# Kernel tuning notes

Hardware: AMD Instinct MI355X
Metric: run time of the kernel (lower is better)

## Reference

```python
import jax, jax.numpy as jnp
import numpy as np

CHUNK_SIZE = 2048
LOCAL_WINDOW = 384
CHUNK_LEN = CHUNK_SIZE - LOCAL_WINDOW  # 1664
N_HEADS = 16
N_KV_HEADS = 4
HEAD_DIM = 128
HIDDEN = 2048
SEQ = 3 * CHUNK_LEN  # 4992
NEG_INF = -1e9


def _cos_sin(positions, dim=HEAD_DIM, base=10000.0):
    inv = 1.0 / (base ** (np.arange(0, dim, 2, dtype=np.float64) / dim))
    freqs = np.outer(np.asarray(positions, np.float64), inv)
    emb = np.concatenate([freqs, freqs], axis=-1)
    return jnp.asarray(np.cos(emb), jnp.float32), jnp.asarray(np.sin(emb), jnp.float32)


def setup_inputs() -> dict:
    key = jax.random.key(0)
    ks = jax.random.split(key, 5)
    hidden_states = jax.random.normal(ks[0], (1, SEQ, HIDDEN), jnp.float32) * 0.02
    position_ids = jnp.arange(SEQ, dtype=jnp.int32)[None, :]
    q_cos, q_sin = _cos_sin(np.arange(SEQ))                 # intra rotary (positions mod chunk_len)
    qc_cos, qc_sin = _cos_sin(np.arange(SEQ) + CHUNK_LEN)   # cross-chunk rotary variant
    k_cos, k_sin = _cos_sin(np.arange(SEQ))                 # key rotary (absolute positions)
    kv_dim = N_KV_HEADS * HEAD_DIM
    Wq = jax.random.normal(ks[1], (N_HEADS * HEAD_DIM, HIDDEN), jnp.float32) * 0.02
    Wk = jax.random.normal(ks[2], (kv_dim, HIDDEN), jnp.float32) * 0.02
    Wv = jax.random.normal(ks[3], (kv_dim, HIDDEN), jnp.float32) * 0.02
    Wo = jax.random.normal(ks[4], (HIDDEN, N_HEADS * HEAD_DIM), jnp.float32) * 0.02
    return dict(hidden_states=hidden_states, position_ids=position_ids,
                q_cos=q_cos, q_sin=q_sin, qc_cos=qc_cos, qc_sin=qc_sin,
                k_cos=k_cos, k_sin=k_sin, Wq=Wq, Wk=Wk, Wv=Wv, Wo=Wo)


def _rotate_half(x):
    x1, x2 = jnp.split(x, 2, axis=-1)
    return jnp.concatenate([-x2, x1], axis=-1)


def _rope(x, cos_t, sin_t, pid):
    # x: [b,h,s,d], pid: [b,s] -> cos/sin [b,1,s,d]
    cos = cos_t[pid][:, None]
    sin = sin_t[pid][:, None]
    return x * cos + _rotate_half(x) * sin


def _attn(q, k, v, causal):
    # flash-attn semantics: scale = head_dim**-0.5, returns output and fp32 LSE [b,h,q]
    scale = q.shape[-1] ** -0.5
    s = jnp.einsum('bhqd,bhkd->bhqk', q, k).astype(jnp.float32) * scale
    if causal:
        L, K = s.shape[-2], s.shape[-1]
        mask = jnp.tril(jnp.ones((L, K), bool))
        s = jnp.where(mask, s, NEG_INF)
    lse = jax.nn.logsumexp(s, axis=-1)
    p = jax.nn.softmax(s, axis=-1).astype(q.dtype)
    out = jnp.einsum('bhqk,bhkd->bhqd', p, v)
    return out, lse


def _merge(parts):
    # LSE-weighted merge of partial attention outputs (weights detached, as in torch)
    outs = jnp.stack([p[0] for p in parts])       # [n,b,h,q,d]
    lses = jnp.stack([p[1] for p in parts])       # [n,b,h,q] fp32
    w = jax.lax.stop_gradient(jax.nn.softmax(lses, axis=0))
    return jnp.sum(outs * w[..., None].astype(outs.dtype), axis=0)


def _forward(hidden_states, position_ids, q_cos, q_sin, qc_cos, qc_sin, k_cos, k_sin, Wq, Wk, Wv, Wo):
    b, s, _ = hidden_states.shape
    q = (hidden_states @ Wq.T).reshape(b, s, N_HEADS, HEAD_DIM).transpose(0, 2, 1, 3)
    k = (hidden_states @ Wk.T).reshape(b, s, N_KV_HEADS, HEAD_DIM).transpose(0, 2, 1, 3)
    v = (hidden_states @ Wv.T).reshape(b, s, N_KV_HEADS, HEAD_DIM).transpose(0, 2, 1, 3)

    k = _rope(k, k_cos, k_sin, position_ids)
    pid = position_ids % CHUNK_LEN

    groups = N_HEADS // N_KV_HEADS
    k = jnp.repeat(k, groups, axis=1)
    v = jnp.repeat(v, groups, axis=1)

    n_chunks = s // CHUNK_LEN
    # chunk 0: intra causal only
    q0 = _rope(q[:, :, :CHUNK_LEN], q_cos, q_sin, pid[:, :CHUNK_LEN])
    out0, _ = _attn(q0, k[:, :, :CHUNK_LEN], v[:, :, :CHUNK_LEN], causal=True)
    outs = [out0]
    for i in range(1, n_chunks):
        b0 = i * CHUNK_LEN
        e = b0 + CHUNK_LEN
        qi = q[:, :, b0:e]
        pid_c = pid[:, b0:e]
        parts = [_attn(_rope(qi, q_cos, q_sin, pid_c), k[:, :, b0:e], v[:, :, b0:e], causal=True),
                 _attn(_rope(qi, qc_cos, qc_sin, pid_c), k[:, :, b0 - CHUNK_LEN:b0], v[:, :, b0 - CHUNK_LEN:b0], causal=False)]
        if b0 - CHUNK_LEN > 0:
            pid_i = jnp.full_like(pid_c, CHUNK_LEN - 1)
            parts.append(_attn(_rope(qi, qc_cos, qc_sin, pid_i), k[:, :, :b0 - CHUNK_LEN], v[:, :, :b0 - CHUNK_LEN], causal=False))
        outs.append(_merge(parts))
    attn_out = jnp.concatenate(outs, axis=2)                      # [b,h,s,d]
    attn_out = attn_out.transpose(0, 2, 1, 3).reshape(b, s, -1)   # [b,s,h*d]
    return attn_out @ Wo.T


def reference(hidden_states, position_ids, q_cos, q_sin, qc_cos, qc_sin, k_cos, k_sin, Wq, Wk, Wv, Wo):
    return _forward(hidden_states, position_ids, q_cos, q_sin, qc_cos, qc_sin, k_cos, k_sin, Wq, Wk, Wv, Wo)
```

## Files before the change

### kernel.cpp

```cpp
#include <hip/hip_runtime.h>

typedef unsigned short u16;
typedef unsigned int u32;
typedef __attribute__((ext_vector_type(8))) __bf16 bf16x8;
typedef __attribute__((ext_vector_type(4))) float f32x4;
typedef __attribute__((ext_vector_type(16))) float f32x16;

#define CLEN 1664
#define SEQL 4992
#define NHEADS 16
#define HD 128
#define HID 2048
#define KVD 512
#define SCALE 0.08838834764831845f
#define SCLOG2E 0.12752615142058843f

__device__ __forceinline__ u16 f2bf(float f) {
  union { float f; u32 u; } v; v.f = f;
  u32 u = v.u;
  return (u16)((u + 0x7FFFu + ((u >> 16) & 1u)) >> 16);
}
__device__ __forceinline__ float bf2f(u16 h) {
  union { u32 u; float f; } v; v.u = (u32)h << 16;
  return v.f;
}
__device__ __forceinline__ f32x4 mfma16(bf16x8 a, bf16x8 b, f32x4 c) {
  return __builtin_amdgcn_mfma_f32_16x16x32_bf16(a, b, c, 0, 0, 0);
}
__device__ __forceinline__ f32x16 mfma32(bf16x8 a, bf16x8 b, f32x16 c) {
  return __builtin_amdgcn_mfma_f32_32x32x16_bf16(a, b, c, 0, 0, 0);
}
__device__ __forceinline__ u32 cvtpk(float lo, float hi) {
  u32 r;
  asm("v_cvt_pk_bf16_f32 %0, %1, %2" : "=v"(r) : "v"(lo), "v"(hi));
  return r;
}
__device__ __forceinline__ float exp2v(float x) {
  float r;
  asm("v_exp_f32 %0, %1" : "=v"(r) : "v"(x));
  return r;
}
__device__ __forceinline__ void gload_lds16(const u16* g, u16* l) {
  __builtin_amdgcn_global_load_lds((const __attribute__((address_space(1))) void*)g,
                                   (__attribute__((address_space(3))) void*)l, 16, 0, 0);
}

#define CVT_Q0 2555904
#define CVT_Q1 1048576
#define CVT_Q2 262144
#define CVT_Q3 262144
#define CVT_Q4 1048576
__device__ __forceinline__ void cvt4(const float* s, u16* d, int q) {
  float4 v = *(const float4*)(s + (size_t)q * 4);
  uint2 p;
  p.x = (u32)f2bf(v.x) | ((u32)f2bf(v.y) << 16);
  p.y = (u32)f2bf(v.z) | ((u32)f2bf(v.w) << 16);
  *(uint2*)(d + (size_t)q * 4) = p;
}
__global__ void cvt_all_kernel(const float* __restrict__ hidden, const float* __restrict__ Wq,
                               const float* __restrict__ Wk, const float* __restrict__ Wv,
                               const float* __restrict__ Wo, u16* __restrict__ h_bf,
                               u16* __restrict__ Wqkv, u16* __restrict__ Wo_bf) {
  int q = blockIdx.x * blockDim.x + threadIdx.x;
  if (q < CVT_Q0) { cvt4(hidden, h_bf, q); return; }
  q -= CVT_Q0;
  if (q < CVT_Q1) { cvt4(Wq, Wqkv, q); return; }
  q -= CVT_Q1;
  if (q < CVT_Q2) { cvt4(Wk, Wqkv + 2048 * 2048, q); return; }
  q -= CVT_Q2;
  if (q < CVT_Q3) { cvt4(Wv, Wqkv + 2560 * 2048, q); return; }
  q -= CVT_Q3;
  if (q < CVT_Q4) cvt4(Wo, Wo_bf, q);
}

#define RP_N0 1277952
#define RP_N1 851968
#define RP_N2 425984
#define RP_N3 319488
__device__ __forceinline__ void rope8(const u16* __restrict__ src, u16* __restrict__ dst,
                                      const float* __restrict__ ctab, const float* __restrict__ stab,
                                      int s, int dstrow, int col, int rowlen, int pid, float scl) {
  const int dh = col & 127;
  const bool hih = dh >= 64;
  const u16* rowp = src + (size_t)s * rowlen;
  union { uint4 u; u16 h[8]; } X, P, O;
  X.u = *(const uint4*)(rowp + col);
  P.u = *(const uint4*)(rowp + col + (hih ? -64 : 64));
  const float* cp = ctab + pid * 128 + dh;
  const float* sp = stab + pid * 128 + dh;
#pragma unroll
  for (int j = 0; j < 8; ++j) {
    float v = bf2f(X.h[j]) * cp[j] + (hih ? bf2f(P.h[j]) : -bf2f(P.h[j])) * sp[j];
    O.h[j] = f2bf(v * scl);
  }
  *(uint4*)(dst + (size_t)dstrow * rowlen + col) = O.u;
}
__global__ void rope_all_kernel(const u16* __restrict__ q_tmp, const u16* __restrict__ k_tmp,
                                u16* __restrict__ qa, u16* __restrict__ qb, u16* __restrict__ qf,
                                u16* __restrict__ k_bf, const float* __restrict__ q_cos,
                                const float* __restrict__ q_sin, const float* __restrict__ qc_cos,
                                const float* __restrict__ qc_sin, const float* __restrict__ k_cos,
                                const float* __restrict__ k_sin) {
  int o = blockIdx.x * blockDim.x + threadIdx.x;
  if (o < RP_N0) {
    int r = o >> 8, col = (o & 255) * 8;
    rope8(q_tmp, qa, q_cos, q_sin, r, r, col, 2048, r % CLEN, SCLOG2E);
    return;
  }
  o -= RP_N0;
  if (o < RP_N1) {
    int r = o >> 8, col = (o & 255) * 8, s = CLEN + r;
    rope8(q_tmp, qb, qc_cos, qc_sin, s, r, col, 2048, s % CLEN, SCLOG2E);
    return;
  }
  o -= RP_N1;
  if (o < RP_N2) {
    int r = o >> 8, col = (o & 255) * 8, s = 2 * CLEN + r;
    rope8(q_tmp, qf, qc_cos, qc_sin, s, r, col, 2048, CLEN - 1, SCLOG2E);
    return;
  }
  o -= RP_N2;
  if (o < RP_N3) {
    int r = o >> 6, col = (o & 63) * 8;
    rope8(k_tmp, k_bf, k_cos, k_sin, r, r, col, 512, r, 1.0f);
  }
}

__global__ __launch_bounds__(256) void gemm_qkv(const u16* __restrict__ A, const u16* __restrict__ B,
                                                u16* __restrict__ q_tmp, u16* __restrict__ k_tmp,
                                                u16* __restrict__ vT) {
  __shared__ __align__(16) u16 Al[128 * 64];
  __shared__ __align__(16) u16 Bl[128 * 64];
  const int K = HID;
  const int t = threadIdx.x;
  const int lane = t & 63, wid = t >> 6;
  const int g = lane >> 4, c = lane & 15;
  const int wr = wid >> 1, wc = wid & 1;
  const int bid = blockIdx.x;
  const int wg = (bid & 7) * 117 + (bid >> 3);
  const int m0 = (wg % 39) * 128, n0 = (wg / 39) * 128;

  f32x4 acc[4][4];
#pragma unroll
  for (int m = 0; m < 4; ++m)
#pragma unroll
    for (int n = 0; n < 4; ++n) acc[m][n] = (f32x4){0.f, 0.f, 0.f, 0.f};

  const int scol = (t & 7) * 8;
  for (int k0 = 0; k0 < K; k0 += 64) {
    __syncthreads();
#pragma unroll
    for (int i = 0; i < 4; ++i) {
      const int r = i * 32 + (t >> 3);
      gload_lds16(A + (size_t)(m0 + r) * K + k0 + scol, Al + i * 2048 + wid * 512);
      gload_lds16(B + (size_t)(n0 + r) * K + k0 + scol, Bl + i * 2048 + wid * 512);
    }
    __syncthreads();
#pragma unroll
    for (int kk = 0; kk < 2; ++kk) {
      bf16x8 af[4], bfr[4];
#pragma unroll
      for (int m = 0; m < 4; ++m)
        af[m] = *(const bf16x8*)(Al + (wr * 64 + m * 16 + c) * 64 + kk * 32 + g * 8);
#pragma unroll
      for (int n = 0; n < 4; ++n)
        bfr[n] = *(const bf16x8*)(Bl + (wc * 64 + n * 16 + c) * 64 + kk * 32 + g * 8);
#pragma unroll
      for (int m = 0; m < 4; ++m)
#pragma unroll
        for (int n = 0; n < 4; ++n)
          acc[m][n] = mfma16(af[m], bfr[n], acc[m][n]);
    }
  }
#pragma unroll
  for (int m = 0; m < 4; ++m)
#pragma unroll
    for (int n = 0; n < 4; ++n)
#pragma unroll
      for (int j = 0; j < 4; ++j) {
        const int row = m0 + wr * 64 + m * 16 + 4 * g + j;
        const int col = n0 + wc * 64 + n * 16 + c;
        const float v = acc[m][n][j];
        if (n0 < 2048)       q_tmp[(size_t)row * 2048 + col] = f2bf(v);
        else if (n0 < 2560)  k_tmp[(size_t)row * 512 + (col - 2048)] = f2bf(v);
        else                 vT[(size_t)(col - 2560) * SEQL + row] = f2bf(v);
      }
}

__global__ __launch_bounds__(256) void gemm_o(const u16* __restrict__ A, const u16* __restrict__ B,
                                              float* __restrict__ Cf) {
  __shared__ __align__(16) u16 Al[128 * 64];
  __shared__ __align__(16) u16 Bl[128 * 64];
  const int K = HID, N = HID;
  const int t = threadIdx.x;
  const int lane = t & 63, wid = t >> 6;
  const int g = lane >> 4, c = lane & 15;
  const int wr = wid >> 1, wc = wid & 1;
  const int bid = blockIdx.x;
  const int wg = (bid & 7) * 78 + (bid >> 3);
  const int m0 = (wg % 39) * 128, n0 = (wg / 39) * 128;

  f32x4 acc[4][4];
#pragma unroll
  for (int m = 0; m < 4; ++m)
#pragma unroll
    for (int n = 0; n < 4; ++n) acc[m][n] = (f32x4){0.f, 0.f, 0.f, 0.f};

  const int scol = (t & 7) * 8;
  for (int k0 = 0; k0 < K; k0 += 64) {
    __syncthreads();
#pragma unroll
    for (int i = 0; i < 4; ++i) {
      const int r = i * 32 + (t >> 3);
      gload_lds16(A + (size_t)(m0 + r) * K + k0 + scol, Al + i * 2048 + wid * 512);
      gload_lds16(B + (size_t)(n0 + r) * K + k0 + scol, Bl + i * 2048 + wid * 512);
    }
    __syncthreads();
#pragma unroll
    for (int kk = 0; kk < 2; ++kk) {
      bf16x8 af[4], bfr[4];
#pragma unroll
      for (int m = 0; m < 4; ++m)
        af[m] = *(const bf16x8*)(Al + (wr * 64 + m * 16 + c) * 64 + kk * 32 + g * 8);
#pragma unroll
      for (int n = 0; n < 4; ++n)
        bfr[n] = *(const bf16x8*)(Bl + (wc * 64 + n * 16 + c) * 64 + kk * 32 + g * 8);
#pragma unroll
      for (int m = 0; m < 4; ++m)
#pragma unroll
        for (int n = 0; n < 4; ++n)
          acc[m][n] = mfma16(af[m], bfr[n], acc[m][n]);
    }
  }
#pragma unroll
  for (int m = 0; m < 4; ++m)
#pragma unroll
    for (int n = 0; n < 4; ++n)
#pragma unroll
      for (int j = 0; j < 4; ++j) {
        const int row = m0 + wr * 64 + m * 16 + 4 * g + j;
        const int col = n0 + wc * 64 + n * 16 + c;
        Cf[(size_t)row * N + col] = acc[m][n][j];
      }
}

__global__ __launch_bounds__(512, 4) void attn_kernel(
    const u16* __restrict__ qa, const u16* __restrict__ qbuf, const u16* __restrict__ qf,
    const u16* __restrict__ kbf, const u16* __restrict__ vT,
    u16* __restrict__ Opart, float* __restrict__ lseout) {
  __shared__ __align__(16) u16 smem[2 * 16384];

  const int t = threadIdx.x, wid = t >> 6, lane = t & 63;
  const int ql = lane & 31, hi = lane >> 5;
  const int ksr = t >> 4, ksc = t & 15;
  const int vsr = t >> 3, vsc = t & 7;

  const int b = blockIdx.x;
  int chunk, seg, qb, head;
  if (b < 336) {
    head = b & 15;
    const int f = b >> 4;
    const int part = f / 7; qb = f % 7;
    chunk = (part == 0) ? 1 : 2;
    seg = (part == 2) ? 1 : 0;
  } else {
    const int i = b - 336;
    qb = 6 - i / 48;
    const int j = i % 48;
    head = j & 15; chunk = j >> 4; seg = chunk;
  }
  const bool causal = (seg == chunk);
  const int nt = causal ? ((qb == 6) ? 26 : (4 * qb + 4)) : 26;
  const int slot = causal ? 0 : ((chunk - seg == 1) ? 1 : 2);
  const int kvh = head >> 2;
  const int kvbase = seg * CLEN;
  const int qcb = qb * 256 + wid * 32;
  const int qpos = qcb + ql;
  const bool wact = qcb < CLEN;

  const u16* qp; int qoff;
  if (causal)                { qp = qa;   qoff = 0; }
  else if (chunk - seg == 1) { qp = qbuf; qoff = CLEN; }
  else                       { qp = qf;   qoff = 2 * CLEN; }

  bf16x8 aq[8];
  {
    const int qrow = wact ? (chunk * CLEN + qpos - qoff) : 0;
    const u16* qptr = qp + (size_t)qrow * HID + head * HD + hi * 8;
#pragma unroll
    for (int ck = 0; ck < 8; ++ck) aq[ck] = *(const bf16x8*)(qptr + ck * 16);
  }

  float l_r = 0.f;
  f32x16 oacc[4];
#pragma unroll
  for (int db = 0; db < 4; ++db)
#pragma unroll
    for (int r = 0; r < 16; ++r) oacc[db][r] = 0.f;

  auto stage = [&](int bb, int kt) {
    const int kv0 = kt * 64;
#pragma unroll
    for (int i = 0; i < 2; ++i) {
      const int rr = ksr + 32 * i;
      const int gs = ksc ^ (rr & 7);
      gload_lds16(kbf + (size_t)(kvbase + kv0 + rr) * KVD + kvh * HD + gs * 8,
                  smem + bb * 16384 + i * 4096 + wid * 512);
    }
#pragma unroll
    for (int i = 0; i < 2; ++i) {
      const int rr = vsr + 64 * i;
      const int gs = vsc ^ (rr & 7);
      gload_lds16(vT + (size_t)(kvh * HD + rr) * SEQL + kvbase + kv0 + gs * 8,
                  smem + bb * 16384 + 8192 + i * 4096 + wid * 512);
    }
  };

  stage(0, 0);
  int cur = 0;
  for (int kt = 0; kt < nt; ++kt) {
    if (kt + 1 < nt) {
      stage(cur ^ 1, kt + 1);
      asm volatile("s_waitcnt vmcnt(4)" ::: "memory");
    } else {
      asm volatile("s_waitcnt vmcnt(0)" ::: "memory");
    }
    __builtin_amdgcn_s_barrier();
    const int kv0 = kt * 64;
    const u16* Kb = smem + cur * 16384;
    const u16* Vb = smem + cur * 16384 + 8192;
#pragma unroll
    for (int s = 0; s < 2; ++s) {
      if (wact && !(causal && kv0 + 32 * s > qcb + 31)) {
        f32x16 sacc;
#pragma unroll
        for (int r = 0; r < 16; ++r) sacc[r] = 0.f;
        const int kr = 32 * s + ql;
        const int r7 = lane & 7;
        __builtin_amdgcn_s_setprio(1);
#pragma unroll
        for (int ck = 0; ck < 8; ++ck) {
          bf16x8 kb = *(const bf16x8*)(Kb + kr * 128 + (((2 * ck + hi) ^ r7) * 8));
          sacc = mfma32(kb, aq[ck], sacc);
        }
        __builtin_amdgcn_s_setprio(0);
        const int thr = qpos - kv0 - 32 * s - 4 * hi;
        float e[16];
        float rs = 0.f;
#pragma unroll
        for (int r = 0; r < 16; ++r) {
          const int crow_r = (r & 3) + 8 * (r >> 2);
          float ev = (causal && crow_r > thr) ? -1e30f : sacc[r];
          e[r] = exp2v(ev);
          rs += e[r];
        }
        rs += __shfl_xor(rs, 32);
        l_r += rs;
        u32 wp[8];
#pragma unroll
        for (int j = 0; j < 8; ++j) wp[j] = cvtpk(e[2 * j], e[2 * j + 1]);
        __builtin_amdgcn_s_setprio(1);
#pragma unroll
        for (int ks = 0; ks < 2; ++ks) {
          union { uint4 u; bf16x8 v; } pa;
          pa.u.x = wp[4 * ks]; pa.u.y = wp[4 * ks + 1];
          pa.u.z = wp[4 * ks + 2]; pa.u.w = wp[4 * ks + 3];
          const int g4a = 8 * s + 4 * ks + hi;
          const int sw = (lane & 7) << 1;
#pragma unroll
          for (int db = 0; db < 4; ++db) {
            const int vrow = 32 * db + ql;
            const uint2 v0 = *(const uint2*)(Vb + vrow * 64 + ((g4a ^ sw) * 4));
            const uint2 v1 = *(const uint2*)(Vb + vrow * 64 + (((g4a + 2) ^ sw) * 4));
            union { uint4 u; bf16x8 v; } bv;
            bv.u.x = v0.x; bv.u.y = v0.y; bv.u.z = v1.x; bv.u.w = v1.y;
            oacc[db] = mfma32(pa.v, bv.v, oacc[db]);
          }
        }
        __builtin_amdgcn_s_setprio(0);
      }
    }
    __builtin_amdgcn_s_barrier();
    cur ^= 1;
  }
  if (wact) {
    const float linv = 1.0f / l_r;
    u16* scr = smem + wid * 4096;
#pragma unroll
    for (int r = 0; r < 16; ++r) {
      const int rrow = (r & 3) + 8 * (r >> 2) + 4 * hi;
      const float li = __shfl(linv, rrow);
#pragma unroll
      for (int db = 0; db < 4; ++db)
        scr[rrow * 128 + db * 32 + ql] = f2bf(oacc[db][r] * li);
    }
    asm volatile("s_waitcnt lgkmcnt(0)" ::: "memory");
    const int rcol = lane & 15;
#pragma unroll
    for (int p = 0; p < 8; ++p) {
      const int row = p * 4 + (lane >> 4);
      uint4 v = *(const uint4*)(scr + row * 128 + rcol * 8);
      const size_t grow = (size_t)(chunk * CLEN + qcb + row);
      *(uint4*)(Opart + ((size_t)slot * SEQL + grow) * HID + head * HD + rcol * 8) = v;
    }
    if (hi == 0)
      lseout[((size_t)slot * NHEADS + head) * SEQL + chunk * CLEN + qcb + ql] = __logf(l_r);
  }
}

__global__ void merge_kernel(const u16* __restrict__ Opart, const float* __restrict__ lse,
                             u16* __restrict__ amrg) {
  const int idx = blockIdx.x * blockDim.x + threadIdx.x;
  const int row = idx >> 8;
  const int col = (idx & 255) * 8;
  const int head = col >> 7;
  const int np = row / CLEN + 1;
  float ls[3];
  float mx = -1e30f;
  for (int i = 0; i < np; ++i) {
    ls[i] = lse[((size_t)i * NHEADS + head) * SEQL + row];
    mx = fmaxf(mx, ls[i]);
  }
  float wsum = 0.f;
  for (int i = 0; i < np; ++i) { ls[i] = __expf(ls[i] - mx); wsum += ls[i]; }
  const float inv = 1.0f / wsum;
  float acc[8];
#pragma unroll
  for (int j = 0; j < 8; ++j) acc[j] = 0.f;
  for (int i = 0; i < np; ++i) {
    union { uint4 u; u16 h[8]; } X;
    X.u = *(const uint4*)(Opart + ((size_t)i * SEQL + row) * (size_t)HID + col);
#pragma unroll
    for (int j = 0; j < 8; ++j) acc[j] += ls[i] * bf2f(X.h[j]);
  }
  union { uint4 u; u16 h[8]; } O;
#pragma unroll
  for (int j = 0; j < 8; ++j) O.h[j] = f2bf(acc[j] * inv);
  *(uint4*)(amrg + (size_t)row * 2048 + col) = O.u;
}

extern "C" void kernel_launch(void* const* d_in, const int* in_sizes, int n_in,
                              void* d_out, int out_size, void* d_ws, size_t ws_size,
                              hipStream_t stream) {
  (void)in_sizes; (void)n_in; (void)out_size; (void)ws_size;
  const float* hidden = (const float*)d_in[0];
  const float* q_cos = (const float*)d_in[2];
  const float* q_sin = (const float*)d_in[3];
  const float* qc_cos = (const float*)d_in[4];
  const float* qc_sin = (const float*)d_in[5];
  const float* k_cos = (const float*)d_in[6];
  const float* k_sin = (const float*)d_in[7];
  const float* Wq = (const float*)d_in[8];
  const float* Wk = (const float*)d_in[9];
  const float* Wv = (const float*)d_in[10];
  const float* Wo = (const float*)d_in[11];
  float* out = (float*)d_out;

  char* ws = (char*)d_ws;
  u16* Wo_bf = (u16*)(ws + 0);
  u16* qa    = (u16*)(ws + 8388608);
  u16* qb    = (u16*)(ws + 28835840);
  u16* qf    = (u16*)(ws + 42467328);
  u16* k_bf  = (u16*)(ws + 49283072);
  u16* vT    = (u16*)(ws + 54394880);
  char* BIG  = ws + 59506688;
  u16* h_bf  = (u16*)(BIG + 0);
  u16* Wqkv  = (u16*)(BIG + 20447232);
  u16* q_tmp = (u16*)(BIG + 33030144);
  u16* k_tmp = (u16*)(BIG + 53477376);
  u16* Opart = (u16*)(BIG + 0);
  float* lse = (float*)(BIG + 61341696);
  u16* amrg  = qa;

  cvt_all_kernel<<<dim3(20224), dim3(256), 0, stream>>>(hidden, Wq, Wk, Wv, Wo, h_bf, Wqkv, Wo_bf);
  gemm_qkv<<<dim3(936), 256, 0, stream>>>(h_bf, Wqkv, q_tmp, k_tmp, vT);
  rope_all_kernel<<<dim3(11232), dim3(256), 0, stream>>>(q_tmp, k_tmp, qa, qb, qf, k_bf,
                                                         q_cos, q_sin, qc_cos, qc_sin, k_cos, k_sin);
  attn_kernel<<<dim3(672), dim3(512), 0, stream>>>(qa, qb, qf, k_bf, vT, Opart, lse);
  merge_kernel<<<dim3(SEQL), dim3(256), 0, stream>>>(Opart, lse, amrg);
  gemm_o<<<dim3(624), 256, 0, stream>>>(amrg, Wo_bf, out);
}
```

Measured before the change: 502.1 us.

## Enlarge attention blocks to 1024 threads with triple-buffered K/V staging

The attention kernel now uses 16 waves per block, covering 512 query rows instead of 256, and the grid drops from 672 to 384 blocks. Each staged K/V tile is therefore shared by twice as many query rows, which cuts global K/V traffic. The double-buffered LDS pipeline becomes a three-stage ring with matching vmcnt waits, so loads run further ahead of compute. The costs are 96 KB of LDS per block, which likely limits a CU to one block, and worse load balance: the last band keeps only 4 of its 16 waves busy, and 384 blocks fill the CUs unevenly.

```diff
diff --git a/kernel.cpp b/kernel.cpp
--- a/kernel.cpp
+++ b/kernel.cpp
@@ -244,11 +244,11 @@
       }
 }
 
-__global__ __launch_bounds__(512, 4) void attn_kernel(
+__global__ __launch_bounds__(1024, 4) void attn_kernel(
     const u16* __restrict__ qa, const u16* __restrict__ qbuf, const u16* __restrict__ qf,
     const u16* __restrict__ kbf, const u16* __restrict__ vT,
     u16* __restrict__ Opart, float* __restrict__ lseout) {
-  __shared__ __align__(16) u16 smem[2 * 16384];
+  __shared__ __align__(16) u16 smem[3 * 16384];
 
   const int t = threadIdx.x, wid = t >> 6, lane = t & 63;
   const int ql = lane & 31, hi = lane >> 5;
@@ -256,25 +256,25 @@
   const int vsr = t >> 3, vsc = t & 7;
 
   const int b = blockIdx.x;
-  int chunk, seg, qb, head;
-  if (b < 336) {
-    head = b & 15;
-    const int f = b >> 4;
-    const int part = f / 7; qb = f % 7;
-    chunk = (part == 0) ? 1 : 2;
-    seg = (part == 2) ? 1 : 0;
+  const int head = b & 15;
+  const int rk = b >> 4;
+  int chunk, seg, band;
+  if (rk < 12) {
+    const int type = rk >> 2;
+    band = rk & 3;
+    chunk = (type == 0) ? 1 : 2;
+    seg = (type == 2) ? 1 : 0;
   } else {
-    const int i = b - 336;
-    qb = 6 - i / 48;
-    const int j = i % 48;
-    head = j & 15; chunk = j >> 4; seg = chunk;
+    const int j = rk - 12;
+    band = 3 - j / 3;
+    chunk = j % 3; seg = chunk;
   }
   const bool causal = (seg == chunk);
-  const int nt = causal ? ((qb == 6) ? 26 : (4 * qb + 4)) : 26;
+  const int nt = causal ? ((band == 3) ? 26 : 8 * (band + 1)) : 26;
   const int slot = causal ? 0 : ((chunk - seg == 1) ? 1 : 2);
   const int kvh = head >> 2;
   const int kvbase = seg * CLEN;
-  const int qcb = qb * 256 + wid * 32;
+  const int qcb = band * 512 + wid * 32;
   const int qpos = qcb + ql;
   const bool wact = qcb < CLEN;
 
@@ -298,37 +298,31 @@
 #pragma unroll
     for (int r = 0; r < 16; ++r) oacc[db][r] = 0.f;
 
-  auto stage = [&](int bb, int kt) {
+  auto stage = [&](int p, int kt) {
     const int kv0 = kt * 64;
-#pragma unroll
-    for (int i = 0; i < 2; ++i) {
-      const int rr = ksr + 32 * i;
-      const int gs = ksc ^ (rr & 7);
-      gload_lds16(kbf + (size_t)(kvbase + kv0 + rr) * KVD + kvh * HD + gs * 8,
-                  smem + bb * 16384 + i * 4096 + wid * 512);
-    }
-#pragma unroll
-    for (int i = 0; i < 2; ++i) {
-      const int rr = vsr + 64 * i;
-      const int gs = vsc ^ (rr & 7);
-      gload_lds16(vT + (size_t)(kvh * HD + rr) * SEQL + kvbase + kv0 + gs * 8,
-                  smem + bb * 16384 + 8192 + i * 4096 + wid * 512);
-    }
+    const int gsk = ksc ^ (ksr & 7);
+    gload_lds16(kbf + (size_t)(kvbase + kv0 + ksr) * KVD + kvh * HD + gsk * 8,
+                smem + p * 16384 + wid * 512);
+    const int gsv = vsc ^ (vsr & 7);
+    gload_lds16(vT + (size_t)(kvh * HD + vsr) * SEQL + kvbase + kv0 + gsv * 8,
+                smem + p * 16384 + 8192 + wid * 512);
   };
 
   stage(0, 0);
-  int cur = 0;
+  stage(1, 1 < nt ? 1 : 0);
   for (int kt = 0; kt < nt; ++kt) {
-    if (kt + 1 < nt) {
-      stage(cur ^ 1, kt + 1);
+    if (kt + 2 < nt) {
+      stage((kt + 2) % 3, kt + 2);
       asm volatile("s_waitcnt vmcnt(4)" ::: "memory");
+    } else if (kt + 1 < nt) {
+      asm volatile("s_waitcnt vmcnt(2)" ::: "memory");
     } else {
       asm volatile("s_waitcnt vmcnt(0)" ::: "memory");
     }
     __builtin_amdgcn_s_barrier();
     const int kv0 = kt * 64;
-    const u16* Kb = smem + cur * 16384;
-    const u16* Vb = smem + cur * 16384 + 8192;
+    const u16* Kb = smem + (kt % 3) * 16384;
+    const u16* Vb = Kb + 8192;
 #pragma unroll
     for (int s = 0; s < 2; ++s) {
       if (wact && !(causal && kv0 + 32 * s > qcb + 31)) {
@@ -381,31 +375,34 @@
       }
     }
     __builtin_amdgcn_s_barrier();
-    cur ^= 1;
-  }
-  if (wact) {
-    const float linv = 1.0f / l_r;
-    u16* scr = smem + wid * 4096;
-#pragma unroll
-    for (int r = 0; r < 16; ++r) {
-      const int rrow = (r & 3) + 8 * (r >> 2) + 4 * hi;
-      const float li = __shfl(linv, rrow);
-#pragma unroll
-      for (int db = 0; db < 4; ++db)
-        scr[rrow * 128 + db * 32 + ql] = f2bf(oacc[db][r] * li);
-    }
-    asm volatile("s_waitcnt lgkmcnt(0)" ::: "memory");
-    const int rcol = lane & 15;
-#pragma unroll
-    for (int p = 0; p < 8; ++p) {
-      const int row = p * 4 + (lane >> 4);
-      uint4 v = *(const uint4*)(scr + row * 128 + rcol * 8);
-      const size_t grow = (size_t)(chunk * CLEN + qcb + row);
-      *(uint4*)(Opart + ((size_t)slot * SEQL + grow) * HID + head * HD + rcol * 8) = v;
-    }
-    if (hi == 0)
-      lseout[((size_t)slot * NHEADS + head) * SEQL + chunk * CLEN + qcb + ql] = __logf(l_r);
-  }
+  }
+  const float linv = wact ? (1.0f / l_r) : 0.f;
+  const int rcol = lane & 15;
+#pragma unroll
+  for (int ph = 0; ph < 2; ++ph) {
+    __syncthreads();
+    if ((wid >> 3) == ph && wact) {
+      u16* scr = smem + (wid & 7) * 4096;
+#pragma unroll
+      for (int r = 0; r < 16; ++r) {
+        const int rrow = (r & 3) + 8 * (r >> 2) + 4 * hi;
+        const float li = __shfl(linv, rrow);
+#pragma unroll
+        for (int db = 0; db < 4; ++db)
+          scr[rrow * 128 + db * 32 + ql] = f2bf(oacc[db][r] * li);
+      }
+      asm volatile("s_waitcnt lgkmcnt(0)" ::: "memory");
+#pragma unroll
+      for (int p = 0; p < 8; ++p) {
+        const int row = p * 4 + (lane >> 4);
+        uint4 v = *(const uint4*)(scr + row * 128 + rcol * 8);
+        const size_t grow = (size_t)(chunk * CLEN + qcb + row);
+        *(uint4*)(Opart + ((size_t)slot * SEQL + grow) * HID + head * HD + rcol * 8) = v;
+      }
+    }
+  }
+  if (wact && hi == 0)
+    lseout[((size_t)slot * NHEADS + head) * SEQL + chunk * CLEN + qcb + ql] = __logf(l_r);
 }
 
 __global__ void merge_kernel(const u16* __restrict__ Opart, const float* __restrict__ lse,
@@ -476,7 +473,7 @@
   gemm_qkv<<<dim3(936), 256, 0, stream>>>(h_bf, Wqkv, q_tmp, k_tmp, vT);
   rope_all_kernel<<<dim3(11232), dim3(256), 0, stream>>>(q_tmp, k_tmp, qa, qb, qf, k_bf,
                                                          q_cos, q_sin, qc_cos, qc_sin, k_cos, k_sin);
-  attn_kernel<<<dim3(672), dim3(512), 0, stream>>>(qa, qb, qf, k_bf, vT, Opart, lse);
+  attn_kernel<<<dim3(384), dim3(1024), 0, stream>>>(qa, qb, qf, k_bf, vT, Opart, lse);
   merge_kernel<<<dim3(SEQL), dim3(256), 0, stream>>>(Opart, lse, amrg);
   gemm_o<<<dim3(624), 256, 0, stream>>>(amrg, Wo_bf, out);
 }
```

Measured after the change: 641.1 us. 27.7% more time.

## Retile QKV GEMM to 256x256 blocks with double-buffered LDS prefetch

Applied to the files above, without the earlier changes.

The QKV projection GEMM moves from 128x128 tiles with 4 waves to 256x256 tiles with 8 waves. The next K-tile is prefetched into a second LDS buffer while the current one is consumed, so a single barrier per step replaces the two-barrier load/compute cycle. MFMA sections get raised priority, and a row bound check covers the padded final M tile, since 5120 exceeds 4992. Only 240 blocks are launched, which may underfill the 256 CUs, and the larger LDS and register footprint lowers occupancy.

```diff
diff --git a/kernel.cpp b/kernel.cpp
--- a/kernel.cpp
+++ b/kernel.cpp
@@ -126,64 +126,94 @@
   }
 }
 
-__global__ __launch_bounds__(256) void gemm_qkv(const u16* __restrict__ A, const u16* __restrict__ B,
+__global__ __launch_bounds__(512) void gemm_qkv(const u16* __restrict__ A, const u16* __restrict__ B,
                                                 u16* __restrict__ q_tmp, u16* __restrict__ k_tmp,
                                                 u16* __restrict__ vT) {
-  __shared__ __align__(16) u16 Al[128 * 64];
-  __shared__ __align__(16) u16 Bl[128 * 64];
+  __shared__ __align__(16) u16 Al[2][256 * 64];
+  __shared__ __align__(16) u16 Bl[2][256 * 64];
   const int K = HID;
   const int t = threadIdx.x;
   const int lane = t & 63, wid = t >> 6;
   const int g = lane >> 4, c = lane & 15;
-  const int wr = wid >> 1, wc = wid & 1;
+  const int wm = wid >> 2, wn = wid & 3;
   const int bid = blockIdx.x;
-  const int wg = (bid & 7) * 117 + (bid >> 3);
-  const int m0 = (wg % 39) * 128, n0 = (wg / 39) * 128;
-
-  f32x4 acc[4][4];
-#pragma unroll
-  for (int m = 0; m < 4; ++m)
-#pragma unroll
-    for (int n = 0; n < 4; ++n) acc[m][n] = (f32x4){0.f, 0.f, 0.f, 0.f};
-
+  const int wg = (bid & 7) * 30 + (bid >> 3);
+  const int m0 = (wg % 20) * 256, n0 = (wg / 20) * 256;
+
+  f32x4 acc[8][4];
+#pragma unroll
+  for (int mf = 0; mf < 8; ++mf)
+#pragma unroll
+    for (int nf = 0; nf < 4; ++nf) acc[mf][nf] = (f32x4){0.f, 0.f, 0.f, 0.f};
+
+  const int srow = t >> 3;
   const int scol = (t & 7) * 8;
-  for (int k0 = 0; k0 < K; k0 += 64) {
-    __syncthreads();
-#pragma unroll
-    for (int i = 0; i < 4; ++i) {
-      const int r = i * 32 + (t >> 3);
-      gload_lds16(A + (size_t)(m0 + r) * K + k0 + scol, Al + i * 2048 + wid * 512);
-      gload_lds16(B + (size_t)(n0 + r) * K + k0 + scol, Bl + i * 2048 + wid * 512);
-    }
-    __syncthreads();
-#pragma unroll
-    for (int kk = 0; kk < 2; ++kk) {
-      bf16x8 af[4], bfr[4];
-#pragma unroll
-      for (int m = 0; m < 4; ++m)
-        af[m] = *(const bf16x8*)(Al + (wr * 64 + m * 16 + c) * 64 + kk * 32 + g * 8);
-#pragma unroll
-      for (int n = 0; n < 4; ++n)
-        bfr[n] = *(const bf16x8*)(Bl + (wc * 64 + n * 16 + c) * 64 + kk * 32 + g * 8);
-#pragma unroll
-      for (int m = 0; m < 4; ++m)
-#pragma unroll
-        for (int n = 0; n < 4; ++n)
-          acc[m][n] = mfma16(af[m], bfr[n], acc[m][n]);
-    }
-  }
-#pragma unroll
-  for (int m = 0; m < 4; ++m)
-#pragma unroll
-    for (int n = 0; n < 4; ++n)
+
+  auto stgA = [&](int buf, int kt, int i) {
+    gload_lds16(A + (size_t)(m0 + i * 64 + srow) * K + kt * 64 + scol,
+                &Al[buf][i * 4096 + wid * 512]);
+  };
+  auto stgB = [&](int buf, int kt, int i) {
+    gload_lds16(B + (size_t)(n0 + i * 64 + srow) * K + kt * 64 + scol,
+                &Bl[buf][i * 4096 + wid * 512]);
+  };
+
+#pragma unroll
+  for (int i = 0; i < 4; ++i) { stgA(0, 0, i); stgB(0, 0, i); }
+
+  const int NT = K / 64;
+  for (int kt = 0; kt < NT; ++kt) {
+    const int buf = kt & 1, nb = buf ^ 1;
+    const bool nx = (kt + 1 < NT);
+#pragma unroll
+    for (int ph = 0; ph < 4; ++ph) {
+      if (nx) {
+        if (ph < 2) { stgA(nb, kt + 1, 2 * ph); stgA(nb, kt + 1, 2 * ph + 1); }
+        else        { stgB(nb, kt + 1, 2 * (ph - 2)); stgB(nb, kt + 1, 2 * (ph - 2) + 1); }
+      }
+      if (ph == 0) {
+        if (nx) asm volatile("s_waitcnt vmcnt(2)" ::: "memory");
+        else    asm volatile("s_waitcnt vmcnt(0)" ::: "memory");
+        __builtin_amdgcn_s_barrier();
+      }
+      const int mfa = 2 * ph;
+      bf16x8 af[2][2], bfr[4][2];
+#pragma unroll
+      for (int q2 = 0; q2 < 2; ++q2)
+#pragma unroll
+        for (int ks = 0; ks < 2; ++ks)
+          af[q2][ks] = *(const bf16x8*)(&Al[buf][(wm * 128 + (mfa + q2) * 16 + c) * 64 + ks * 32 + g * 8]);
+#pragma unroll
+      for (int nf = 0; nf < 4; ++nf)
+#pragma unroll
+        for (int ks = 0; ks < 2; ++ks)
+          bfr[nf][ks] = *(const bf16x8*)(&Bl[buf][(wn * 64 + nf * 16 + c) * 64 + ks * 32 + g * 8]);
+      __builtin_amdgcn_s_setprio(1);
+#pragma unroll
+      for (int q2 = 0; q2 < 2; ++q2)
+#pragma unroll
+        for (int nf = 0; nf < 4; ++nf)
+#pragma unroll
+          for (int ks = 0; ks < 2; ++ks)
+            acc[mfa + q2][nf] = mfma16(af[q2][ks], bfr[nf][ks], acc[mfa + q2][nf]);
+      __builtin_amdgcn_s_setprio(0);
+    }
+    __builtin_amdgcn_s_barrier();
+  }
+#pragma unroll
+  for (int mf = 0; mf < 8; ++mf)
+#pragma unroll
+    for (int nf = 0; nf < 4; ++nf)
 #pragma unroll
       for (int j = 0; j < 4; ++j) {
-        const int row = m0 + wr * 64 + m * 16 + 4 * g + j;
-        const int col = n0 + wc * 64 + n * 16 + c;
-        const float v = acc[m][n][j];
-        if (n0 < 2048)       q_tmp[(size_t)row * 2048 + col] = f2bf(v);
-        else if (n0 < 2560)  k_tmp[(size_t)row * 512 + (col - 2048)] = f2bf(v);
-        else                 vT[(size_t)(col - 2560) * SEQL + row] = f2bf(v);
+        const int row = m0 + wm * 128 + mf * 16 + 4 * g + j;
+        const int col = n0 + wn * 64 + nf * 16 + c;
+        if (row < SEQL) {
+          const float v = acc[mf][nf][j];
+          if (col < 2048)       q_tmp[(size_t)row * 2048 + col] = f2bf(v);
+          else if (col < 2560)  k_tmp[(size_t)row * 512 + (col - 2048)] = f2bf(v);
+          else                  vT[(size_t)(col - 2560) * SEQL + row] = f2bf(v);
+        }
       }
 }
 
@@ -358,7 +388,7 @@
         l_r += rs;
         u32 wp[8];
 #pragma unroll
-        for (int j = 0; j < 8; ++j) wp[j] = cvtpk(e[2 * j], e[2 * j + 1]);
+        for (int j2 = 0; j2 < 8; ++j2) wp[j2] = cvtpk(e[2 * j2], e[2 * j2 + 1]);
         __builtin_amdgcn_s_setprio(1);
 #pragma unroll
         for (int ks = 0; ks < 2; ++ks) {
@@ -473,7 +503,7 @@
   u16* amrg  = qa;
 
   cvt_all_kernel<<<dim3(20224), dim3(256), 0, stream>>>(hidden, Wq, Wk, Wv, Wo, h_bf, Wqkv, Wo_bf);
-  gemm_qkv<<<dim3(936), 256, 0, stream>>>(h_bf, Wqkv, q_tmp, k_tmp, vT);
+  gemm_qkv<<<dim3(240), dim3(512), 0, stream>>>(h_bf, Wqkv, q_tmp, k_tmp, vT);
   rope_all_kernel<<<dim3(11232), dim3(256), 0, stream>>>(q_tmp, k_tmp, qa, qb, qf, k_bf,
                                                          q_cos, q_sin, qc_cos, qc_sin, k_cos, k_sin);
   attn_kernel<<<dim3(672), dim3(512), 0, stream>>>(qa, qb, qf, k_bf, vT, Opart, lse);
```

Measured after the change: 517.8 us. +3.1%, slower.

## Fuse query RoPE into attention kernel, keep separate key RoPE pass

Applied to the files above, without the earlier changes.

Query rotary embedding, with the softmax scale folded in, is now applied inside the attention kernel as each wave loads its Q fragment from the un-roped projection output. The three materialised roped-Q buffers and their write/read traffic go away, and the standalone rope kernel now handles only keys. In exchange, each attention block reads cos/sin tables and does extra per-lane arithmetic before its main loop, and the workspace layout is shrunk and reshuffled.

```diff
diff --git a/kernel.cpp b/kernel.cpp
--- a/kernel.cpp
+++ b/kernel.cpp
@@ -73,57 +73,26 @@
   if (q < CVT_Q4) cvt4(Wo, Wo_bf, q);
 }
 
-#define RP_N0 1277952
-#define RP_N1 851968
-#define RP_N2 425984
-#define RP_N3 319488
-__device__ __forceinline__ void rope8(const u16* __restrict__ src, u16* __restrict__ dst,
-                                      const float* __restrict__ ctab, const float* __restrict__ stab,
-                                      int s, int dstrow, int col, int rowlen, int pid, float scl) {
+#define RPK_N 319488
+__global__ void rope_k_kernel(const u16* __restrict__ k_tmp, u16* __restrict__ k_bf,
+                              const float* __restrict__ k_cos, const float* __restrict__ k_sin) {
+  int o = blockIdx.x * blockDim.x + threadIdx.x;
+  if (o >= RPK_N) return;
+  const int r = o >> 6, col = (o & 63) * 8;
   const int dh = col & 127;
   const bool hih = dh >= 64;
-  const u16* rowp = src + (size_t)s * rowlen;
+  const u16* rowp = k_tmp + (size_t)r * 512;
   union { uint4 u; u16 h[8]; } X, P, O;
   X.u = *(const uint4*)(rowp + col);
   P.u = *(const uint4*)(rowp + col + (hih ? -64 : 64));
-  const float* cp = ctab + pid * 128 + dh;
-  const float* sp = stab + pid * 128 + dh;
+  const float* cp = k_cos + r * 128 + dh;
+  const float* sp = k_sin + r * 128 + dh;
 #pragma unroll
   for (int j = 0; j < 8; ++j) {
     float v = bf2f(X.h[j]) * cp[j] + (hih ? bf2f(P.h[j]) : -bf2f(P.h[j])) * sp[j];
-    O.h[j] = f2bf(v * scl);
-  }
-  *(uint4*)(dst + (size_t)dstrow * rowlen + col) = O.u;
-}
-__global__ void rope_all_kernel(const u16* __restrict__ q_tmp, const u16* __restrict__ k_tmp,
-                                u16* __restrict__ qa, u16* __restrict__ qb, u16* __restrict__ qf,
-                                u16* __restrict__ k_bf, const float* __restrict__ q_cos,
-                                const float* __restrict__ q_sin, const float* __restrict__ qc_cos,
-                                const float* __restrict__ qc_sin, const float* __restrict__ k_cos,
-                                const float* __restrict__ k_sin) {
-  int o = blockIdx.x * blockDim.x + threadIdx.x;
-  if (o < RP_N0) {
-    int r = o >> 8, col = (o & 255) * 8;
-    rope8(q_tmp, qa, q_cos, q_sin, r, r, col, 2048, r % CLEN, SCLOG2E);
-    return;
-  }
-  o -= RP_N0;
-  if (o < RP_N1) {
-    int r = o >> 8, col = (o & 255) * 8, s = CLEN + r;
-    rope8(q_tmp, qb, qc_cos, qc_sin, s, r, col, 2048, s % CLEN, SCLOG2E);
-    return;
-  }
-  o -= RP_N1;
-  if (o < RP_N2) {
-    int r = o >> 8, col = (o & 255) * 8, s = 2 * CLEN + r;
-    rope8(q_tmp, qf, qc_cos, qc_sin, s, r, col, 2048, CLEN - 1, SCLOG2E);
-    return;
-  }
-  o -= RP_N2;
-  if (o < RP_N3) {
-    int r = o >> 6, col = (o & 63) * 8;
-    rope8(k_tmp, k_bf, k_cos, k_sin, r, r, col, 512, r, 1.0f);
-  }
+    O.h[j] = f2bf(v);
+  }
+  *(uint4*)(k_bf + (size_t)r * 512 + col) = O.u;
 }
 
 __global__ __launch_bounds__(256) void gemm_qkv(const u16* __restrict__ A, const u16* __restrict__ B,
@@ -245,8 +214,9 @@
 }
 
 __global__ __launch_bounds__(512, 4) void attn_kernel(
-    const u16* __restrict__ qa, const u16* __restrict__ qbuf, const u16* __restrict__ qf,
-    const u16* __restrict__ kbf, const u16* __restrict__ vT,
+    const u16* __restrict__ q_tmp, const u16* __restrict__ kbf, const u16* __restrict__ vT,
+    const float* __restrict__ q_cos, const float* __restrict__ q_sin,
+    const float* __restrict__ qc_cos, const float* __restrict__ qc_sin,
     u16* __restrict__ Opart, float* __restrict__ lseout) {
   __shared__ __align__(16) u16 smem[2 * 16384];
 
@@ -278,17 +248,30 @@
   const int qpos = qcb + ql;
   const bool wact = qcb < CLEN;
 
-  const u16* qp; int qoff;
-  if (causal)                { qp = qa;   qoff = 0; }
-  else if (chunk - seg == 1) { qp = qbuf; qoff = CLEN; }
-  else                       { qp = qf;   qoff = 2 * CLEN; }
-
   bf16x8 aq[8];
   {
-    const int qrow = wact ? (chunk * CLEN + qpos - qoff) : 0;
-    const u16* qptr = qp + (size_t)qrow * HID + head * HD + hi * 8;
-#pragma unroll
-    for (int ck = 0; ck < 8; ++ck) aq[ck] = *(const bf16x8*)(qptr + ck * 16);
+    const float* ct = causal ? q_cos : qc_cos;
+    const float* st = causal ? q_sin : qc_sin;
+    const int pid = (causal || (chunk - seg == 1)) ? qpos : (CLEN - 1);
+    const int qrow = wact ? (chunk * CLEN + qpos) : 0;
+    const u16* qptr = q_tmp + (size_t)qrow * HID + head * HD + hi * 8;
+    union { bf16x8 v; u16 h[8]; } xf[8];
+#pragma unroll
+    for (int ck = 0; ck < 8; ++ck) xf[ck].v = *(const bf16x8*)(qptr + ck * 16);
+    const float* cb = ct + pid * 128 + hi * 8;
+    const float* sb = st + pid * 128 + hi * 8;
+#pragma unroll
+    for (int ck = 0; ck < 8; ++ck) {
+      union { bf16x8 v; u16 h[8]; } o;
+      const int d0 = ck * 16;
+      const float sgn = (ck < 4) ? -1.f : 1.f;
+#pragma unroll
+      for (int j = 0; j < 8; ++j) {
+        float v = bf2f(xf[ck].h[j]) * cb[d0 + j] + sgn * bf2f(xf[ck ^ 4].h[j]) * sb[d0 + j];
+        o.h[j] = f2bf(v * SCLOG2E);
+      }
+      aq[ck] = o.v;
+    }
   }
 
   float l_r = 0.f;
@@ -358,7 +341,7 @@
         l_r += rs;
         u32 wp[8];
 #pragma unroll
-        for (int j = 0; j < 8; ++j) wp[j] = cvtpk(e[2 * j], e[2 * j + 1]);
+        for (int j2 = 0; j2 < 8; ++j2) wp[j2] = cvtpk(e[2 * j2], e[2 * j2 + 1]);
         __builtin_amdgcn_s_setprio(1);
 #pragma unroll
         for (int ks = 0; ks < 2; ++ks) {
@@ -458,25 +441,22 @@
 
   char* ws = (char*)d_ws;
   u16* Wo_bf = (u16*)(ws + 0);
-  u16* qa    = (u16*)(ws + 8388608);
-  u16* qb    = (u16*)(ws + 28835840);
-  u16* qf    = (u16*)(ws + 42467328);
-  u16* k_bf  = (u16*)(ws + 49283072);
-  u16* vT    = (u16*)(ws + 54394880);
-  char* BIG  = ws + 59506688;
+  u16* q_tmp = (u16*)(ws + 8388608);
+  u16* k_bf  = (u16*)(ws + 28835840);
+  u16* vT    = (u16*)(ws + 33947648);
+  char* BIG  = ws + 39059456;
   u16* h_bf  = (u16*)(BIG + 0);
   u16* Wqkv  = (u16*)(BIG + 20447232);
-  u16* q_tmp = (u16*)(BIG + 33030144);
-  u16* k_tmp = (u16*)(BIG + 53477376);
+  u16* k_tmp = (u16*)(BIG + 33030144);
   u16* Opart = (u16*)(BIG + 0);
   float* lse = (float*)(BIG + 61341696);
-  u16* amrg  = qa;
+  u16* amrg  = q_tmp;
 
   cvt_all_kernel<<<dim3(20224), dim3(256), 0, stream>>>(hidden, Wq, Wk, Wv, Wo, h_bf, Wqkv, Wo_bf);
   gemm_qkv<<<dim3(936), 256, 0, stream>>>(h_bf, Wqkv, q_tmp, k_tmp, vT);
-  rope_all_kernel<<<dim3(11232), dim3(256), 0, stream>>>(q_tmp, k_tmp, qa, qb, qf, k_bf,
-                                                         q_cos, q_sin, qc_cos, qc_sin, k_cos, k_sin);
-  attn_kernel<<<dim3(672), dim3(512), 0, stream>>>(qa, qb, qf, k_bf, vT, Opart, lse);
+  rope_k_kernel<<<dim3(1248), dim3(256), 0, stream>>>(k_tmp, k_bf, k_cos, k_sin);
+  attn_kernel<<<dim3(672), dim3(512), 0, stream>>>(q_tmp, k_bf, vT, q_cos, q_sin,
+                                                   qc_cos, qc_sin, Opart, lse);
   merge_kernel<<<dim3(SEQL), dim3(256), 0, stream>>>(Opart, lse, amrg);
   gemm_o<<<dim3(624), 256, 0, stream>>>(amrg, Wo_bf, out);
 }
```

Result: no change. 501.9 us (-0.0%).
